# Performance work log

Measured on AMD Instinct MI355X. Metric: run time of the kernel, lower is better.

## Reference

```python
import jax, jax.numpy as jnp
import numpy as np

# Loihi neuron constants (from a typical slayerSNN network.yaml)
I_DECAY = 1024.0   # current decay (of 4096)
V_DECAY = 128.0    # voltage decay (of 4096)
THETA = 100.0      # firing threshold


def spike_loihi(x):
    """Loihi CUBA neuron dynamics over trailing time axis. x: [..., T] weighted input."""
    xT = jnp.moveaxis(x, -1, 0)  # [T, ...]
    a_i = (4096.0 - I_DECAY) / 4096.0
    a_v = (4096.0 - V_DECAY) / 4096.0

    def step(carry, xt):
        u, v = carry
        u = a_i * u + xt           # synaptic current
        v = a_v * v + u            # membrane voltage
        s = (v >= THETA).astype(x.dtype)
        v = v * (1.0 - s)          # reset on spike
        return (u, v), s

    z = jnp.zeros(xT.shape[1:], x.dtype)
    _, s = jax.lax.scan(step, (z, z), xT)
    return jnp.moveaxis(s, 0, -1)


def delay_shift(x):
    """Shift spikes by 1 timestep along last axis (slayer.delayShift(spike, 1))."""
    return jnp.concatenate([jnp.zeros_like(x[..., :1]), x[..., :-1]], axis=-1)


def conv_t(x, w):
    """Per-timestep 2D conv, padding 1. x: [N,C,H,W,T], w: [O,I,3,3]."""
    N, C, H, W, T = x.shape
    xt = jnp.transpose(x, (0, 4, 1, 2, 3)).reshape(N * T, C, H, W)
    y = jax.lax.conv_general_dilated(xt, w, (1, 1), [(1, 1), (1, 1)],
                                     dimension_numbers=('NCHW', 'OIHW', 'NCHW'))
    O = w.shape[0]
    return jnp.transpose(y.reshape(N, T, O, H, W), (0, 2, 3, 4, 1))


def sum_pool2(x, w):
    """slayer.pool(2): 2x2 sum-pool scaled by (loaded) scalar pool weight."""
    N, C, H, W, T = x.shape
    return x.reshape(N, C, H // 2, 2, W // 2, 2, T).sum(axis=(3, 5)) * w


def setup_inputs() -> dict:
    key = jax.random.key(0)
    ks = jax.random.split(key, 8)
    N, T = 16, 128
    spike = jax.random.bernoulli(ks[0], 0.1, (N, 2, 40, 40, T)).astype(jnp.float32)
    conv1_w = jax.random.normal(ks[1], (8, 2, 3, 3), jnp.float32) * 0.5
    conv2_w = jax.random.normal(ks[2], (16, 8, 3, 3), jnp.float32) * 0.05
    conv3_w = jax.random.normal(ks[3], (32, 16, 3, 3), jnp.float32) * 0.05
    fc1_w = jax.random.normal(ks[4], (512, 10 * 10 * 32), jnp.float32) * 0.02
    pool1_w = jnp.asarray(1.1, jnp.float32)
    pool2_w = jnp.asarray(1.1, jnp.float32)
    return {"spike": spike, "conv1_w": conv1_w, "conv2_w": conv2_w,
            "conv3_w": conv3_w, "pool1_w": pool1_w, "pool2_w": pool2_w,
            "fc1_w": fc1_w}


def reference(spike, conv1_w, conv2_w, conv3_w, pool1_w, pool2_w, fc1_w):
    x = spike_loihi(conv_t(spike, conv1_w * 20.0))    # weightScale=20
    x = delay_shift(x)
    x = spike_loihi(sum_pool2(x, pool1_w))
    x = delay_shift(x)
    x = spike_loihi(conv_t(x, conv2_w * 100.0))       # weightScale=100
    x = delay_shift(x)
    x = spike_loihi(sum_pool2(x, pool2_w))
    x = delay_shift(x)
    x = spike_loihi(conv_t(x, conv3_w * 100.0))       # weightScale=100
    N, T = x.shape[0], x.shape[-1]
    x = x.reshape(N, -1, 1, 1, T)                     # [N, 3200, 1, 1, T]
    x = delay_shift(x)
    x = spike_loihi(jnp.einsum('nchwt,oc->nohwt', x, fc1_w))
    x = delay_shift(x)
    return x
```

## Files before the change

### kernel.cpp

```cpp
#include <hip/hip_runtime.h>
#include <stdint.h>


#define T 128
#define AI 0.75f
#define AV 0.96875f
#define THETA 100.0f

typedef __attribute__((ext_vector_type(8))) short v8s;
typedef __attribute__((ext_vector_type(16))) float v16f;

__device__ __forceinline__ void neuron_step(float x, float& u, float& v, float& s) {
    u = AI * u + x;
    v = AV * v + u;
    s = (v >= THETA) ? 1.0f : 0.0f;
    v = v * (1.0f - s);
}

__global__ __launch_bounds__(256) void conv1_scan(
    const float* __restrict__ in, const float* __restrict__ cw,
    uint8_t* __restrict__ sout)
{
    __shared__ float ldsF[64 * 130];
    int bid0 = blockIdx.x;
    int bid = (bid0 & 7) * 400 + (bid0 >> 3);
    int wg = bid % 5;
    int hy = (bid / 5) % 40;
    int n  = bid / 200;
    int tid = threadIdx.x;
    int wxl = tid >> 5, tt = tid & 31, t0 = tt * 4;
    int wx = wg * 8 + wxl;

    float4 tap[18];
    #pragma unroll
    for (int c = 0; c < 2; c++)
      #pragma unroll
      for (int dh = 0; dh < 3; dh++)
        #pragma unroll
        for (int dw = 0; dw < 3; dw++) {
            int q = c * 9 + dh * 3 + dw;
            int hh = hy + dh - 1, ww = wx + dw - 1;
            bool ok = (hh >= 0) && (hh < 40) && (ww >= 0) && (ww < 40);
            tap[q] = ok ? *(const float4*)(in +
                (((size_t)(n * 2 + c) * 40 + hh) * 40 + ww) * T + t0)
                        : make_float4(0.f, 0.f, 0.f, 0.f);
        }

    #pragma unroll
    for (int o = 0; o < 8; o++) {
        const float* wp = cw + o * 18;
        float a0 = 0.f, a1 = 0.f, a2 = 0.f, a3 = 0.f;
        #pragma unroll
        for (int q = 0; q < 18; q++) {
            a0 += wp[q] * tap[q].x;  a1 += wp[q] * tap[q].y;
            a2 += wp[q] * tap[q].z;  a3 += wp[q] * tap[q].w;
        }
        float* xr = &ldsF[(o * 8 + wxl) * 130 + t0];
        xr[0] = a0 * 20.0f; xr[1] = a1 * 20.0f;
        xr[2] = a2 * 20.0f; xr[3] = a3 * 20.0f;
    }
    __syncthreads();
    if (tid < 64) {
        int o = tid >> 3, wxl2 = tid & 7;
        float u = 0.f, v = 0.f;
        uint32_t ob[32];
        const float* xr = &ldsF[tid * 130];
        #pragma unroll
        for (int tb = 0; tb < 32; tb++) {
            float s0, s1, s2, s3;
            neuron_step(xr[tb * 4 + 0], u, v, s0);
            neuron_step(xr[tb * 4 + 1], u, v, s1);
            neuron_step(xr[tb * 4 + 2], u, v, s2);
            neuron_step(xr[tb * 4 + 3], u, v, s3);
            ob[tb] = (uint32_t)s0 | ((uint32_t)s1 << 8) |
                     ((uint32_t)s2 << 16) | ((uint32_t)s3 << 24);
        }
        uint32_t* op = (uint32_t*)(sout +
            (((size_t)(n * 8 + o) * 40 + hy) * 40 + wg * 8 + wxl2) * T);
        #pragma unroll
        for (int k = 0; k < 8; k++)
            *(uint4*)&op[k * 4] =
                make_uint4(ob[k*4], ob[k*4+1], ob[k*4+2], ob[k*4+3]);
    }
}

template<int C, int HO, int WO>
__global__ __launch_bounds__(320) void pool_pad(
    const uint8_t* __restrict__ in, const float* __restrict__ pw_ptr,
    uint16_t* __restrict__ sP)
{
    constexpr int CB = 320 / C;
    constexpr int GP = (HO * WO) / CB;
    __shared__ uint8_t raw[320 * 132];
    uint32_t* ldsF = (uint32_t*)raw;
    uint8_t*  sbuf = raw;

    int bid = blockIdx.x;
    int grp = bid % GP, n = bid / GP;
    int tid = threadIdx.x;
    float pw = pw_ptr[0];

    float u = 0.f, v = 0.f;
    uint32_t ob[32];
    uint32_t carry = 0;

    #pragma unroll
    for (int tb = 0; tb < 2; tb++) {
        __syncthreads();
        #pragma unroll
        for (int k = 0; k < 4; k++) {
            int f = tid + k * 320;
            int row = f >> 2, q = f & 3;
            int c = row / CB, p = row % CB;
            int hw = grp * CB + p;
            int wx = hw % WO, hy = hw / WO;
            const uint8_t* p00 = in +
                (((size_t)(n * C + c) * (2 * HO) + 2 * hy) * (2 * WO) + 2 * wx) * T;
            int off = tb * 64 + q * 16;
            uint4 a = *(const uint4*)(p00 + off);
            uint4 b = *(const uint4*)(p00 + T + off);
            uint4 cc = *(const uint4*)(p00 + 2 * WO * T + off);
            uint4 d = *(const uint4*)(p00 + 2 * WO * T + T + off);
            *(uint4*)&ldsF[row * 20 + q * 4] =
                make_uint4(a.x + b.x + cc.x + d.x, a.y + b.y + cc.y + d.y,
                           a.z + b.z + cc.z + d.z, a.w + b.w + cc.w + d.w);
        }
        __syncthreads();
        #pragma unroll
        for (int q = 0; q < 4; q++) {
            uint4 w = *(const uint4*)&ldsF[tid * 20 + q * 4];
            uint32_t words[4] = {w.x, w.y, w.z, w.w};
            #pragma unroll
            for (int j = 0; j < 4; j++) {
                uint32_t cur = words[j];
                uint32_t del = (cur << 8) | carry;
                carry = cur >> 24;
                float s0, s1, s2, s3;
                neuron_step(pw * (float)(del & 0xffu),         u, v, s0);
                neuron_step(pw * (float)((del >> 8) & 0xffu),  u, v, s1);
                neuron_step(pw * (float)((del >> 16) & 0xffu), u, v, s2);
                neuron_step(pw * (float)((del >> 24) & 0xffu), u, v, s3);
                ob[tb * 16 + q * 4 + j] = (uint32_t)s0 | ((uint32_t)s1 << 8) |
                                          ((uint32_t)s2 << 16) | ((uint32_t)s3 << 24);
            }
        }
    }

    __syncthreads();
    #pragma unroll
    for (int j = 0; j < 32; j++)
        *(uint32_t*)&sbuf[tid * 132 + j * 4] = ob[j];
    __syncthreads();

    constexpr int CHK = CB * 128;
    #pragma unroll
    for (int k = 0; k < CHK / 320; k++) {
        int ci = k * 320 + tid;
        int p = ci >> 7, tau = ci & 127;
        int hw = grp * CB + p;
        int wx = hw % WO, hy = hw / WO;
        uint32_t wb[8];
        #pragma unroll
        for (int e = 0; e < 16; e += 2) {
            uint32_t lo = 0u, hi = 0u;
            if (tau >= 1) {
                if (e < C)     lo = sbuf[(e * CB + p) * 132 + tau - 1] ? 0x3F80u : 0u;
                if (e + 1 < C) hi = sbuf[((e + 1) * CB + p) * 132 + tau - 1] ? 0x3F80u : 0u;
            }
            wb[e >> 1] = lo | (hi << 16);
        }
        uint16_t* dst = sP + ((size_t)((n * (HO + 2) + hy + 1) * (WO + 2)
                                       + wx + 1)) * 2048 + tau * 16;
        *(uint4*)dst       = make_uint4(wb[0], wb[1], wb[2], wb[3]);
        *(uint4*)(dst + 8) = make_uint4(wb[4], wb[5], wb[6], wb[7]);
    }
}

__global__ __launch_bounds__(256) void prep(
    const float* __restrict__ fw, const float* __restrict__ c2w,
    const float* __restrict__ c3w, uint16_t* __restrict__ bs,
    uint16_t* __restrict__ apk, uint16_t* __restrict__ s2P,
    uint16_t* __restrict__ s4P)
{
    int bid = blockIdx.x;
    int tid = threadIdx.x;
    if (bid < 1600) {
        int i = bid * 256 + tid;
        float4 wv = *(const float4*)(fw + i * 4);
        float w4[4] = {wv.x, wv.y, wv.z, wv.w};
        uint16_t h[4], m[4], l[4];
        #pragma unroll
        for (int j = 0; j < 4; j++) {
            uint32_t b0 = __float_as_uint(w4[j]);
            h[j] = (uint16_t)(b0 >> 16);
            float r1 = w4[j] - __uint_as_float(b0 & 0xFFFF0000u);
            uint32_t b1 = __float_as_uint(r1);
            m[j] = (uint16_t)(b1 >> 16);
            float r2 = r1 - __uint_as_float(b1 & 0xFFFF0000u);
            l[j] = (uint16_t)(__float_as_uint(r2) >> 16);
        }
        *(ushort4*)(bs +       0 + i * 4) = make_ushort4(h[0], h[1], h[2], h[3]);
        *(ushort4*)(bs + 1638400 + i * 4) = make_ushort4(m[0], m[1], m[2], m[3]);
        *(ushort4*)(bs + 3276800 + i * 4) = make_ushort4(l[0], l[1], l[2], l[3]);
    } else if (bid < 1614) {
        int unit = (bid - 1600) * 4 + (tid >> 6);
        if (unit >= 54) return;
        int conv = unit / 27;
        int plane = (unit % 27) / 9;
        int dlt = unit % 9;
        int lane = tid & 63;
        int o = lane & 31, chi = (lane >> 5) * 8;
        int CO = conv ? 32 : 16;
        int CI = conv ? 16 : 8;
        const float* Wp = conv ? c3w : c2w;
        uint32_t wb[4] = {0u, 0u, 0u, 0u};
        #pragma unroll
        for (int e = 0; e < 8; e++) {
            int c = chi + e;
            float w = (o < CO && c < CI) ? Wp[((size_t)o * CI + c) * 9 + dlt] : 0.f;
            uint32_t b0 = __float_as_uint(w);
            uint16_t hi = (uint16_t)(b0 >> 16);
            float r1 = w - __uint_as_float(b0 & 0xFFFF0000u);
            uint32_t b1 = __float_as_uint(r1);
            uint16_t md = (uint16_t)(b1 >> 16);
            float r2 = r1 - __uint_as_float(b1 & 0xFFFF0000u);
            uint16_t lo = (uint16_t)(__float_as_uint(r2) >> 16);
            uint32_t pv = (plane == 0) ? hi : ((plane == 1) ? md : lo);
            wb[e >> 1] |= pv << ((e & 1) * 16);
        }
        *(uint4*)(apk + ((size_t)conv * 27 + plane * 9 + dlt) * 512 + lane * 8) =
            make_uint4(wb[0], wb[1], wb[2], wb[3]);
    } else {
        int hid = bid - 1614;
        uint8_t* dst;
        if (hid < 1344) {
            int n = hid / 84, r = hid % 84;
            int hy, wx;
            if (r < 22)      { hy = 0;  wx = r; }
            else if (r < 44) { hy = 21; wx = r - 22; }
            else { int r2 = r - 44; hy = 1 + (r2 >> 1); wx = (r2 & 1) ? 21 : 0; }
            dst = (uint8_t*)s2P + ((size_t)(n * 484) + hy * 22 + wx) * 4096;
        } else {
            int h2 = hid - 1344;
            int n = h2 / 44, r = h2 % 44;
            int hy, wx;
            if (r < 12)      { hy = 0;  wx = r; }
            else if (r < 24) { hy = 11; wx = r - 12; }
            else { int r2 = r - 24; hy = 1 + (r2 >> 1); wx = (r2 & 1) ? 11 : 0; }
            dst = (uint8_t*)s4P + ((size_t)(n * 144) + hy * 12 + wx) * 4096;
        }
        *(uint4*)(dst + tid * 16) = make_uint4(0u, 0u, 0u, 0u);
    }
}

template<int COUT, int PB, int H, int W>
__global__ __launch_bounds__(256, 2) void conv_scan_mfma(
    const uint16_t* __restrict__ sP, const uint16_t* __restrict__ apk,
    float scale, uint8_t* __restrict__ sout)
{
    constexpr int ROWS = COUT * PB;
    __shared__ float ldsF[ROWS * 130];
    constexpr int HW = H * W;
    constexpr int GP = HW / PB;
    int per = (16 * GP) >> 3;
    int vbid = (blockIdx.x & 7) * per + (blockIdx.x >> 3);
    int n = vbid / GP, grp = vbid % GP;
    int tid = threadIdx.x;
    int wv = tid >> 6, lane = tid & 63;
    int l31 = lane & 31, lhi = lane >> 5;
    int t0 = wv * 32;

    const uint16_t* ap = apk + (size_t)lane * 8;
    v8s a0[9], a1[9], a2[9];
    #pragma unroll
    for (int d = 0; d < 9; d++) {
        a0[d] = *(const v8s*)(ap + d * 512);
        a1[d] = *(const v8s*)(ap + (9 + d) * 512);
        a2[d] = *(const v8s*)(ap + (18 + d) * 512);
    }

    #pragma unroll
    for (int p = 0; p < PB; p++) {
        int hw = grp * PB + p;
        int hy = hw / W, wx = hw % W;
        v8s bfr[9];
        #pragma unroll
        for (int d = 0; d < 9; d++) {
            int dh = d / 3, dw = d % 3;
            const uint16_t* src = sP
                + ((size_t)((n * (H + 2) + hy + dh) * (W + 2) + wx + dw)) * 2048
                + (t0 + l31) * 16 + lhi * 8;
            bfr[d] = *(const v8s*)src;
        }
        v16f ac0, ac1, ac2;
        #pragma unroll
        for (int e = 0; e < 16; e++) { ac0[e] = 0.f; ac1[e] = 0.f; ac2[e] = 0.f; }
        #pragma unroll
        for (int d = 0; d < 9; d++) {
            ac0 = __builtin_amdgcn_mfma_f32_32x32x16_bf16(a0[d], bfr[d], ac0, 0, 0, 0);
            ac1 = __builtin_amdgcn_mfma_f32_32x32x16_bf16(a1[d], bfr[d], ac1, 0, 0, 0);
            ac2 = __builtin_amdgcn_mfma_f32_32x32x16_bf16(a2[d], bfr[d], ac2, 0, 0, 0);
        }
        constexpr int NR = (COUT == 32) ? 16 : 8;
        #pragma unroll
        for (int r = 0; r < NR; r++) {
            int o = (r & 3) + 8 * (r >> 2) + 4 * lhi;
            ldsF[(o * PB + p) * 130 + t0 + l31] =
                (ac0[r] + ac1[r] + ac2[r]) * scale;
        }
    }
    __syncthreads();
    if (tid < ROWS) {
        int o = tid / PB, p = tid % PB;
        int hw = grp * PB + p;
        float u = 0.f, v = 0.f;
        uint32_t ob[32];
        const float* xr = &ldsF[tid * 130];
        #pragma unroll
        for (int tb = 0; tb < 32; tb++) {
            float2 xa = *(const float2*)(xr + tb * 4);
            float2 xb = *(const float2*)(xr + tb * 4 + 2);
            float s0, s1, s2, s3;
            neuron_step(xa.x, u, v, s0); neuron_step(xa.y, u, v, s1);
            neuron_step(xb.x, u, v, s2); neuron_step(xb.y, u, v, s3);
            ob[tb] = (uint32_t)s0 | ((uint32_t)s1 << 8) |
                     ((uint32_t)s2 << 16) | ((uint32_t)s3 << 24);
        }
        uint32_t* op = (uint32_t*)(sout + ((size_t)(n * COUT + o) * HW + hw) * 128);
        #pragma unroll
        for (int k = 0; k < 8; k++)
            *(uint4*)&op[k * 4] =
                make_uint4(ob[k*4], ob[k*4+1], ob[k*4+2], ob[k*4+3]);
    }
}

__global__ __launch_bounds__(256) void sT_bf16(
    const uint8_t* __restrict__ s5, uint16_t* __restrict__ At)
{
    __shared__ uint8_t tile[64 * 132];
    int bid = blockIdx.x;
    int n = bid / 50;
    int c0 = (bid % 50) * 64;
    int tid = threadIdx.x;
    {
        int row = tid >> 2, q = tid & 3;
        const uint8_t* src = s5 + ((size_t)(n * 3200 + c0 + row)) * T + q * 32;
        *(uint4*)&tile[row * 132 + q * 32]      = *(const uint4*)src;
        *(uint4*)&tile[row * 132 + q * 32 + 16] = *(const uint4*)(src + 16);
    }
    __syncthreads();
    int t = tid >> 1, half = tid & 1;
    uint32_t wb[16];
    if (t == 0) {
        #pragma unroll
        for (int j = 0; j < 16; j++) wb[j] = 0u;
    } else {
        #pragma unroll
        for (int j = 0; j < 16; j++) {
            uint32_t lo = tile[(half * 32 + 2 * j) * 132 + (t - 1)] ? 0x3F80u : 0u;
            uint32_t hi = tile[(half * 32 + 2 * j + 1) * 132 + (t - 1)] ? 0x3F80u : 0u;
            wb[j] = lo | (hi << 16);
        }
    }
    uint16_t* dst = At + ((size_t)(n * 128 + t)) * 3200 + c0 + half * 32;
    #pragma unroll
    for (int k = 0; k < 4; k++)
        *(uint4*)(dst + k * 8) = make_uint4(wb[k*4], wb[k*4+1], wb[k*4+2], wb[k*4+3]);
}

#define GLDS16(g, s) __builtin_amdgcn_global_load_lds( \
    (const __attribute__((address_space(1))) uint32_t*)(g), \
    (__attribute__((address_space(3))) uint32_t*)(s), 16, 0, 0)

__global__ __launch_bounds__(512, 4) void fc_gemm_mfma(
    const uint16_t* __restrict__ At,
    const uint16_t* __restrict__ Bs,
    float* __restrict__ ypart)
{
    __shared__ uint8_t lds[65536];
    int bid0 = blockIdx.x;
    int bid = (bid0 & 7) * 80 + (bid0 >> 3);
    int n  = bid & 15;
    int ob = (bid >> 4) & 3;
    int ks = bid >> 6;
    int o0 = ob * 128;
    int cbase = ks * 320;

    int tid = threadIdx.x;
    int w8 = tid >> 6;
    int wm = w8 >> 2;
    int wn = w8 & 3;
    int lane = tid & 63;
    int l31 = lane & 31;
    int lhi = lane >> 5;
    int rb = lane >> 3;
    int gsw = (lane & 7) ^ (rb & 7);

    v16f acc[2];
    #pragma unroll
    for (int mi = 0; mi < 2; mi++)
        #pragma unroll
        for (int e = 0; e < 16; e++) acc[mi][e] = 0.0f;

    const uint16_t* Abase = At + (size_t)(n * 128) * 3200 + gsw * 8;

    for (int kc = 0; kc < 5; kc++) {
        int c0 = cbase + kc * 64;
        #pragma unroll
        for (int i = 0; i < 2; i++) {
            int cid = i * 8 + w8;
            const uint16_t* src = Abase + (size_t)(cid * 8 + rb) * 3200 + c0;
            GLDS16(src, lds + cid * 1024);
        }
        #pragma unroll
        for (int j = 0; j < 6; j++) {
            int cid = j * 8 + w8;
            int f0 = cid * 1024;
            int s = f0 >> 14;
            int r = ((f0 & 16383) >> 7) + rb;
            const uint16_t* src = Bs + (size_t)(s * 512 + o0 + r) * 3200
                                     + c0 + gsw * 8;
            GLDS16(src, lds + 16384 + f0);
        }
        __syncthreads();
        #pragma unroll
        for (int kf = 0; kf < 4; kf++) {
            int gc = kf * 2 + lhi;
            v8s av[2];
            #pragma unroll
            for (int mi = 0; mi < 2; mi++) {
                int t = wm * 64 + mi * 32 + l31;
                av[mi] = *(const v8s*)(lds + t * 128 + ((gc ^ (t & 7)) << 4));
            }
            #pragma unroll
            for (int s = 0; s < 3; s++) {
                int r = wn * 32 + l31;
                v8s bv = *(const v8s*)(lds + 16384 + s * 16384 + r * 128
                                       + ((gc ^ (r & 7)) << 4));
                #pragma unroll
                for (int mi = 0; mi < 2; mi++)
                    acc[mi] = __builtin_amdgcn_mfma_f32_32x32x16_bf16(
                        av[mi], bv, acc[mi], 0, 0, 0);
            }
        }
        __syncthreads();
    }
    float* yp = ypart + (size_t)ks * 1048576 + (size_t)n * 65536;
    int o = o0 + wn * 32 + l31;
    #pragma unroll
    for (int mi = 0; mi < 2; mi++) {
        #pragma unroll
        for (int r = 0; r < 16; r++) {
            int trow = wm * 64 + mi * 32 + (r & 3) + 8 * (r >> 2) + 4 * lhi;
            yp[trow * 512 + o] = acc[mi][r];
        }
    }
}

__global__ __launch_bounds__(64) void fc_scan(
    const float* __restrict__ yp,
    float* __restrict__ out)
{
    int id = blockIdx.x * 64 + threadIdx.x;
    int o = id & 511;
    int n = id >> 9;
    const float* base = yp + (size_t)n * 65536 + o;
    float u = 0.f, v = 0.f;
    float prev = 0.f;
    for (int tb = 0; tb < T / 4; tb++) {
        float b[4];
        #pragma unroll
        for (int j = 0; j < 4; j++) {
            int t = tb * 4 + j;
            float x = base[(size_t)t * 512];
            #pragma unroll
            for (int k = 1; k < 10; k++)
                x += base[(size_t)k * 1048576 + (size_t)t * 512];
            float s;
            neuron_step(x, u, v, s);
            b[j] = prev; prev = s;
        }
        *(float4*)&out[((size_t)(n * 512 + o)) * T + tb * 4] =
            make_float4(b[0], b[1], b[2], b[3]);
    }
}

extern "C" void kernel_launch(void* const* d_in, const int* in_sizes, int n_in,
                              void* d_out, int out_size, void* d_ws, size_t ws_size,
                              hipStream_t stream) {
    const float* spike = (const float*)d_in[0];
    const float* c1w   = (const float*)d_in[1];
    const float* c2w   = (const float*)d_in[2];
    const float* c3w   = (const float*)d_in[3];
    const float* p1w   = (const float*)d_in[4];
    const float* p2w   = (const float*)d_in[5];
    const float* fcw   = (const float*)d_in[6];
    float* out = (float*)d_out;

    char* ws = (char*)d_ws;
    uint8_t*  s1    = (uint8_t*)(ws);
    uint16_t* Bs16  = (uint16_t*)(ws + 26214400);
    uint16_t* Apk   = (uint16_t*)(ws + 36044800);
    uint16_t* s2P   = (uint16_t*)(ws + 36100096);
    uint8_t*  s3    = (uint8_t*)(ws + 67819520);
    uint16_t* s4P   = (uint16_t*)(ws + 80926720);
    uint8_t*  s5    = (uint8_t*)(ws + 90363904);
    uint16_t* At16  = (uint16_t*)(ws + 96917504);
    float*    ypart = (float*)(ws + 110024704);

    prep<<<3662, 256, 0, stream>>>(fcw, c2w, c3w, Bs16, Apk, s2P, s4P);
    conv1_scan<<<3200, 256, 0, stream>>>(spike, c1w, s1);

    pool_pad<8, 20, 20><<<160, 320, 0, stream>>>(s1, p1w, s2P);
    conv_scan_mfma<16, 4, 20, 20><<<1600, 256, 0, stream>>>(s2P, Apk, 100.0f, s3);

    pool_pad<16, 10, 10><<<80, 320, 0, stream>>>(s3, p2w, s4P);
    conv_scan_mfma<32, 2, 10, 10><<<800, 256, 0, stream>>>(s4P, Apk + 13824, 100.0f, s5);

    sT_bf16<<<800, 256, 0, stream>>>(s5, At16);
    fc_gemm_mfma<<<640, 512, 0, stream>>>(At16, Bs16, ypart);
    fc_scan<<<128, 64, 0, stream>>>(ypart, out);
}
```

Before: 245.4 us.

## Parallelize fc_scan partial-sum reduction across threads via LDS staging

The final scan kernel now has 256 threads per block cooperatively load and sum the ten split-K partials for 16 outputs over all timesteps into shared memory. Only 16 threads then run the serial neuron recurrence from LDS. The goal is more memory-level parallelism and occupancy than the old design, where few threads each issued long serial chains of strided global loads. The scan phase leaves most threads idle, and the grid grows from 128 to 512 blocks.

```diff
diff --git a/kernel.cpp b/kernel.cpp
--- a/kernel.cpp
+++ b/kernel.cpp
@@ -457,31 +457,44 @@
     }
 }
 
-__global__ __launch_bounds__(64) void fc_scan(
+__global__ __launch_bounds__(256) void fc_scan(
     const float* __restrict__ yp,
     float* __restrict__ out)
 {
-    int id = blockIdx.x * 64 + threadIdx.x;
-    int o = id & 511;
-    int n = id >> 9;
-    const float* base = yp + (size_t)n * 65536 + o;
-    float u = 0.f, v = 0.f;
-    float prev = 0.f;
-    for (int tb = 0; tb < T / 4; tb++) {
-        float b[4];
-        #pragma unroll
-        for (int j = 0; j < 4; j++) {
-            int t = tb * 4 + j;
-            float x = base[(size_t)t * 512];
+    __shared__ float ldsX[16 * 132];
+    int b = blockIdx.x;
+    int n = b >> 5;
+    int o0 = (b & 31) * 16;
+    int tid = threadIdx.x;
+    int t16 = tid >> 4, ol = tid & 15;
+    const float* base = yp + (size_t)n * 65536 + o0 + ol;
+
+    #pragma unroll
+    for (int tb = 0; tb < 8; tb++) {
+        int t = tb * 16 + t16;
+        float x = base[(size_t)t * 512];
+        #pragma unroll
+        for (int k = 1; k < 10; k++)
+            x += base[(size_t)k * 1048576 + (size_t)t * 512];
+        ldsX[ol * 132 + t] = x;
+    }
+    __syncthreads();
+    if (tid < 16) {
+        int o = o0 + tid;
+        const float* xr = &ldsX[tid * 132];
+        float u = 0.f, v = 0.f;
+        float prev = 0.f;
+        float* op = out + ((size_t)(n * 512 + o)) * T;
+        for (int tb = 0; tb < 32; tb++) {
+            float bv[4];
             #pragma unroll
-            for (int k = 1; k < 10; k++)
-                x += base[(size_t)k * 1048576 + (size_t)t * 512];
-            float s;
-            neuron_step(x, u, v, s);
-            b[j] = prev; prev = s;
-        }
-        *(float4*)&out[((size_t)(n * 512 + o)) * T + tb * 4] =
-            make_float4(b[0], b[1], b[2], b[3]);
+            for (int j = 0; j < 4; j++) {
+                float s;
+                neuron_step(xr[tb * 4 + j], u, v, s);
+                bv[j] = prev; prev = s;
+            }
+            *(float4*)&op[tb * 4] = make_float4(bv[0], bv[1], bv[2], bv[3]);
+        }
     }
 }
 
@@ -519,5 +532,5 @@
 
     sT_bf16<<<800, 256, 0, stream>>>(s5, At16);
     fc_gemm_mfma<<<640, 512, 0, stream>>>(At16, Bs16, ypart);
-    fc_scan<<<128, 64, 0, stream>>>(ypart, out);
-}
+    fc_scan<<<512, 256, 0, stream>>>(ypart, out);
+}
```

After: 240.8 us. No clear change (-1.9%).
